# Kernel optimization log

Hardware: AMD Instinct MI355X
Metric: run time of the kernel (lower is better)

The kernel has to match this reference:

```python
import jax, jax.numpy as jnp
import numpy as np

NEG_SLOPE = 0.2  # PyG GATConv leaky_relu slope


def _seg_sum(x, seg, n):
    return jax.ops.segment_sum(x, seg, num_segments=n)


def _seg_softmax(e, seg, n):
    # numerically stable softmax over edges grouped by destination node
    m = jax.ops.segment_max(e, seg, num_segments=n)
    w = jnp.exp(e - m[seg])
    s = jax.ops.segment_sum(w, seg, num_segments=n)
    return w / (s[seg] + 1e-16)


def _gat_bipartite(x_src, x_dst, Ws, Wd, a_s, a_d, b, src, dst, H=4, C=32):
    # PyG GATConv((x_src, x_dst), edge_index), concat=True, add_self_loops=False
    n_dst = x_dst.shape[0]
    hs = (x_src @ Ws).reshape(-1, H, C)   # [Ns,H,C]
    hd = (x_dst @ Wd).reshape(-1, H, C)   # [Nd,H,C]
    es = jnp.einsum('nhc,hc->nh', hs, a_s)  # alpha_src per node
    ed = jnp.einsum('nhc,hc->nh', hd, a_d)  # alpha_dst per node
    e = jax.nn.leaky_relu(es[src] + ed[dst], NEG_SLOPE)  # [E,H]
    alpha = _seg_softmax(e, dst, n_dst)                   # softmax per dst
    out = _seg_sum(hs[src] * alpha[..., None], dst, n_dst)  # [Nd,H,C]
    return out.reshape(n_dst, H * C) + b


def _gcn_self_loops(x, W, b, src, dst):
    # PyG GCNConv with add_self_loops=True, symmetric normalization
    n = x.shape[0]
    xw = x @ W
    deg = _seg_sum(jnp.ones_like(dst, dtype=xw.dtype), dst, n) + 1.0  # +1 self loop
    dinv = jax.lax.rsqrt(deg)
    coef = (dinv[src] * dinv[dst])[:, None]
    agg = _seg_sum(xw[src] * coef, dst, n)
    agg = agg + xw * (dinv * dinv)[:, None]  # self-loop contribution
    return agg + b


def setup_inputs() -> dict:
    D, H, C = 128, 4, 32
    Nb, Nc, Nt = 200_000, 20_000, 2_000
    Eadj, Ebc, Ect = 1_600_000, 200_000, 20_000
    key = jax.random.key(0)
    ks = jax.random.split(key, 24)
    g = 1.0 / np.sqrt(D)
    ga = 1.0 / np.sqrt(C)
    inp = {
        'x_building': jax.random.normal(ks[0], (Nb, D), jnp.float32),
        'x_cable': jax.random.normal(ks[1], (Nc, D), jnp.float32),
        'x_transformer': jax.random.normal(ks[2], (Nt, D), jnp.float32),
        'Ws1': jax.random.normal(ks[3], (D, D), jnp.float32) * g,
        'Wd1': jax.random.normal(ks[4], (D, D), jnp.float32) * g,
        'a_s1': jax.random.normal(ks[5], (H, C), jnp.float32) * ga,
        'a_d1': jax.random.normal(ks[6], (H, C), jnp.float32) * ga,
        'b1': jnp.zeros((D,), jnp.float32),
        'Ws2': jax.random.normal(ks[7], (D, D), jnp.float32) * g,
        'Wd2': jax.random.normal(ks[8], (D, D), jnp.float32) * g,
        'a_s2': jax.random.normal(ks[9], (H, C), jnp.float32) * ga,
        'a_d2': jax.random.normal(ks[10], (H, C), jnp.float32) * ga,
        'b2': jnp.zeros((D,), jnp.float32),
        'Wg': jax.random.normal(ks[11], (D, D), jnp.float32) * g,
        'bg': jnp.zeros((D,), jnp.float32),
        'b2c_src': jax.random.randint(ks[12], (Ebc,), 0, Nb, jnp.int32),
        'b2c_dst': jax.random.randint(ks[13], (Ebc,), 0, Nc, jnp.int32),
        'c2t_src': jax.random.randint(ks[14], (Ect,), 0, Nc, jnp.int32),
        'c2t_dst': jax.random.randint(ks[15], (Ect,), 0, Nt, jnp.int32),
        'adj_src': jax.random.randint(ks[16], (Eadj,), 0, Nb, jnp.int32),
        'adj_dst': jax.random.randint(ks[17], (Eadj,), 0, Nb, jnp.int32),
    }
    return inp


def reference(x_building, x_cable, x_transformer,
              Ws1, Wd1, a_s1, a_d1, b1,
              Ws2, Wd2, a_s2, a_d2, b2,
              Wg, bg,
              b2c_src, b2c_dst, c2t_src, c2t_dst, adj_src, adj_dst):
    # building -> cable_group (GAT), residual 0.5
    h_lv = _gat_bipartite(x_building, x_cable, Ws1, Wd1, a_s1, a_d1, b1,
                          b2c_src, b2c_dst)
    h_cable = x_cable + 0.5 * h_lv
    # (updated) cable_group -> transformer (GAT), residual 0.5
    h_tr = _gat_bipartite(h_cable, x_transformer, Ws2, Wd2, a_s2, a_d2, b2,
                          c2t_src, c2t_dst)
    h_transformer = x_transformer + 0.5 * h_tr
    # building adjacency (GCN with self loops), residual 0.2
    h_adj = _gcn_self_loops(x_building, Wg, bg, adj_src, adj_dst)
    h_building = x_building + 0.2 * h_adj
    return (h_building, h_cable, h_transformer)
```

## Files before the change

kernel.cpp:

```cpp
#include <hip/hip_runtime.h>
#include <hip/hip_bf16.h>
#include <stdint.h>

typedef __attribute__((ext_vector_type(8))) short bf16x8;
typedef __attribute__((ext_vector_type(4))) float floatx4;
typedef __attribute__((ext_vector_type(4))) float f32x4;
typedef __attribute__((ext_vector_type(2))) float f32x2;

__device__ __forceinline__ float2 bf2f(uint32_t u) {
  float2 r;
  r.x = __uint_as_float(u << 16);
  r.y = __uint_as_float(u & 0xffff0000u);
  return r;
}
__device__ __forceinline__ uint16_t f2bf(float f) {
  uint32_t u = __float_as_uint(f);
  uint32_t r = (u + 0x7fffu + ((u >> 16) & 1u)) >> 16;
  return (uint16_t)r;
}
__device__ __forceinline__ uint32_t f2bf_pack(float a, float b) {
  return (uint32_t)f2bf(a) | ((uint32_t)f2bf(b) << 16);
}
__device__ __forceinline__ int iclamp(int v, int lo, int hi) {
  return v < lo ? lo : (v > hi ? hi : v);
}
__device__ __forceinline__ float lrelu(float v) { return v >= 0.f ? v : 0.2f * v; }

__device__ __forceinline__ int detect_f32(const uint32_t* __restrict__ det) {
  uint32_t v = det[threadIdx.x & 63];
  int e = (v >> 23) & 0xFF;
  unsigned long long b = __ballot(e >= 90 && e <= 160);
  return __popcll(b) >= 48;
}

__device__ __forceinline__ void acc8(float* a, uint4 r, float w) {
  float2 f0 = bf2f(r.x), f1 = bf2f(r.y), f2 = bf2f(r.z), f3 = bf2f(r.w);
  a[0] += w * f0.x; a[1] += w * f0.y;
  a[2] += w * f1.x; a[3] += w * f1.y;
  a[4] += w * f2.x; a[5] += w * f2.y;
  a[6] += w * f3.x; a[7] += w * f3.y;
}

__global__ void transp_zero(const void* __restrict__ W0, const void* __restrict__ W1,
                            const void* __restrict__ W2, const void* __restrict__ W3,
                            const void* __restrict__ W4, __hip_bfloat16* __restrict__ WT,
                            int* __restrict__ zp, int zn, const uint32_t* __restrict__ det) {
  int isf32 = detect_f32(det);
  int b = blockIdx.x;
  int w = b >> 6;
  int i = (b & 63) * 256 + threadIdx.x;
  const void* W = (w == 0) ? W0 : (w == 1) ? W1 : (w == 2) ? W2 : (w == 3) ? W3 : W4;
  int k = i >> 7, n = i & 127;
  uint16_t h;
  if (isf32)
    h = f2bf(((const float*)W)[i]);
  else
    h = ((const uint16_t*)W)[i];
  ((uint16_t*)WT)[w * 16384 + n * 128 + k] = h;
  for (int j = blockIdx.x * 256 + threadIdx.x; j < zn; j += gridDim.x * 256) zp[j] = 0;
}

__global__ void hist_all(const int* __restrict__ d0, int E0, const int* __restrict__ d1,
                         int E1, const int* __restrict__ d2, int E2,
                         int* __restrict__ cnt, int n0, int n1, int n2) {
  int i = blockIdx.x * 256 + threadIdx.x;
  if (i < E0) {
    atomicAdd(&cnt[iclamp(d0[i], 0, n0 - 1)], 1);
  } else if (i < E0 + E1) {
    int j = i - E0;
    atomicAdd(&cnt[n0 + iclamp(d1[j], 0, n1 - 1)], 1);
  } else if (i < E0 + E1 + E2) {
    int j = i - E0 - E1;
    atomicAdd(&cnt[n0 + n1 + iclamp(d2[j], 0, n2 - 1)], 1);
  }
}

__global__ void scanp_all(const int* __restrict__ cnt, int* __restrict__ off,
                          int* __restrict__ bsum, int n0, int n1, int n2,
                          int nb0, int nb1) {
  int b = blockIdx.x;
  int seg, lb, base, n;
  if (b < nb0) { seg = 0; lb = b; base = 0; n = n0; }
  else if (b < nb0 + nb1) { seg = 1; lb = b - nb0; base = n0; n = n1; }
  else { seg = 2; lb = b - nb0 - nb1; base = n0 + n1; n = n2; }
  const int* in = cnt + base;
  int* out = off + base;
  int* bs = bsum + seg * 256;
  __shared__ int lds[256];
  int t = threadIdx.x;
  int pbase = lb * 1024 + t * 4;
  int v[4];
  int s = 0;
#pragma unroll
  for (int j = 0; j < 4; j++) {
    v[j] = (pbase + j < n) ? in[pbase + j] : 0;
    s += v[j];
  }
  lds[t] = s;
  __syncthreads();
  for (int d = 1; d < 256; d <<= 1) {
    int x = 0;
    if (t >= d) x = lds[t - d];
    __syncthreads();
    if (t >= d) lds[t] += x;
    __syncthreads();
  }
  int run = (t > 0) ? lds[t - 1] : 0;
  if (t == 255) bs[lb] = lds[255];
#pragma unroll
  for (int j = 0; j < 4; j++) {
    if (pbase + j < n) out[pbase + j] = run;
    run += v[j];
  }
}

__global__ void scans_all(int* __restrict__ bsum, int nb0, int nb1, int nb2) {
  int seg = blockIdx.x;
  int nb = (seg == 0) ? nb0 : (seg == 1) ? nb1 : nb2;
  int* bs = bsum + seg * 256;
  __shared__ int lds[256];
  int t = threadIdx.x;
  int v = (t < nb) ? bs[t] : 0;
  lds[t] = v;
  __syncthreads();
  for (int d = 1; d < 256; d <<= 1) {
    int x = 0;
    if (t >= d) x = lds[t - d];
    __syncthreads();
    if (t >= d) lds[t] += x;
    __syncthreads();
  }
  if (t < nb) bs[t] = (t > 0) ? lds[t - 1] : 0;
}

__global__ void scanadd_dinv(int* __restrict__ off, const int* __restrict__ bsum,
                             const int* __restrict__ cnt, float* __restrict__ dinv,
                             int n0, int n1, int n2) {
  int i = blockIdx.x * 256 + threadIdx.x;
  if (i >= n0 + n1 + n2) return;
  int seg, li;
  if (i < n0) { seg = 0; li = i; }
  else if (i < n0 + n1) { seg = 1; li = i - n0; }
  else { seg = 2; li = i - n0 - n1; }
  off[i] += bsum[seg * 256 + (li >> 10)];
  if (seg == 2) dinv[li] = rsqrtf((float)max(cnt[i], 0) + 1.0f);
}

__global__ void fill_all(const int* __restrict__ s0, const int* __restrict__ d0, int E0,
                         const int* __restrict__ s1, const int* __restrict__ d1, int E1,
                         const int* __restrict__ s2, const int* __restrict__ d2, int E2,
                         const int* __restrict__ off, int* __restrict__ cur,
                         int* __restrict__ r0, int* __restrict__ r1, int* __restrict__ r2,
                         int n0, int n1, int n2) {
  int i = blockIdx.x * 256 + threadIdx.x;
  const int* sp;
  const int* dp;
  int* rp;
  int base, N, E, j;
  if (i < E0) { sp = s0; dp = d0; rp = r0; base = 0; N = n0; E = E0; j = i; }
  else if (i < E0 + E1) { sp = s1; dp = d1; rp = r1; base = n0; N = n1; E = E1; j = i - E0; }
  else if (i < E0 + E1 + E2) { sp = s2; dp = d2; rp = r2; base = n0 + n1; N = n2; E = E2; j = i - E0 - E1; }
  else return;
  int d = iclamp(dp[j], 0, N - 1);
  int gi = base + d;
  int p = off[gi] + atomicAdd(&cur[gi], 1);
  rp[iclamp(p, 0, E - 1)] = sp[j];
}

struct MMB {
  const void* A0; const void* A1; const void* A2;
  unsigned long long ao0, ao1, ao2;
  const __hip_bfloat16* W0; const __hip_bfloat16* W1; const __hip_bfloat16* W2;
  __hip_bfloat16* O0; __hip_bfloat16* O1; __hip_bfloat16* O2;
  float* E0; float* E1; float* E2;
  const void* V0; const void* V1; const void* V2;
  int M0, M1, M2, B1, B2;
};

__global__ __launch_bounds__(256) void mm_batch(MMB p, const uint32_t* __restrict__ det) {
  int isf32 = detect_f32(det);
  const void* Abase;
  size_t aoff;
  const __hip_bfloat16* WTp;
  __hip_bfloat16* out;
  float* esp;
  const void* av;
  int M, bRow;
  int bid = (int)blockIdx.x;
  if (bid >= p.B2) {
    Abase = p.A2; aoff = p.ao2; WTp = p.W2; out = p.O2; esp = p.E2; av = p.V2;
    M = p.M2; bRow = bid - p.B2;
  } else if (bid >= p.B1) {
    Abase = p.A1; aoff = p.ao1; WTp = p.W1; out = p.O1; esp = p.E1; av = p.V1;
    M = p.M1; bRow = bid - p.B1;
  } else {
    Abase = p.A0; aoff = p.ao0; WTp = p.W0; out = p.O0; esp = p.E0; av = p.V0;
    M = p.M0; bRow = bid;
  }
  __shared__ __align__(16) __hip_bfloat16 w[128 * 136];
  int tid = threadIdx.x;
  for (int i = tid; i < 2048; i += 256) {
    int row = i >> 4, ch = i & 15;
    *(uint4*)&w[row * 136 + ch * 8] = *(const uint4*)&WTp[row * 128 + ch * 8];
  }
  __syncthreads();
  int wave = tid >> 6, lane = tid & 63;
  int l15 = lane & 15, kq = (lane >> 4) * 8;
  int row0 = bRow * 64 + wave * 16;
  int m = row0 + l15;
  int mc = m < M ? m : M - 1;
  floatx4 acc[8];
#pragma unroll
  for (int t = 0; t < 8; t++) acc[t] = (floatx4){0.f, 0.f, 0.f, 0.f};
#pragma unroll
  for (int k0 = 0; k0 < 128; k0 += 32) {
    union { bf16x8 v; uint32_t u[4]; } au;
    size_t eoff = aoff + (size_t)mc * 128 + k0 + kq;
    if (isf32) {
      const f32x4* Af = (const f32x4*)((const float*)Abase + eoff);
      f32x4 f0 = __builtin_nontemporal_load(Af);
      f32x4 f1 = __builtin_nontemporal_load(Af + 1);
      au.u[0] = f2bf_pack(f0.x, f0.y);
      au.u[1] = f2bf_pack(f0.z, f0.w);
      au.u[2] = f2bf_pack(f1.x, f1.y);
      au.u[3] = f2bf_pack(f1.z, f1.w);
    } else {
      au.v = __builtin_nontemporal_load((const bf16x8*)((const __hip_bfloat16*)Abase + eoff));
    }
#pragma unroll
    for (int t = 0; t < 8; t++) {
      bf16x8 b = *(const bf16x8*)&w[(t * 16 + l15) * 136 + k0 + kq];
      acc[t] = __builtin_amdgcn_mfma_f32_16x16x32_bf16(au.v, b, acc[t], 0, 0, 0);
    }
  }
  int rbase = row0 + (lane >> 4) * 4;
  uint16_t* o16 = (uint16_t*)out;
#pragma unroll
  for (int r = 0; r < 4; r++) {
    int rr = rbase + r;
    if (rr < M) {
#pragma unroll
      for (int t = 0; t < 8; t++) o16[(size_t)rr * 128 + t * 16 + l15] = f2bf(acc[t][r]);
    }
  }
  if (esp) {
    float av8[8];
    if (isf32) {
      const float* af = (const float*)av;
#pragma unroll
      for (int t = 0; t < 8; t++) av8[t] = af[t * 16 + l15];
    } else {
      const uint16_t* ab = (const uint16_t*)av;
#pragma unroll
      for (int t = 0; t < 8; t++) av8[t] = __uint_as_float((uint32_t)ab[t * 16 + l15] << 16);
    }
    float ph[4][4];
#pragma unroll
    for (int h = 0; h < 4; h++)
#pragma unroll
      for (int r = 0; r < 4; r++)
        ph[h][r] = acc[2 * h][r] * av8[2 * h] + acc[2 * h + 1][r] * av8[2 * h + 1];
#pragma unroll
    for (int h = 0; h < 4; h++)
#pragma unroll
      for (int r = 0; r < 4; r++) {
        float v = ph[h][r];
        v += __shfl_xor(v, 1);
        v += __shfl_xor(v, 2);
        v += __shfl_xor(v, 4);
        v += __shfl_xor(v, 8);
        ph[h][r] = v;
      }
    int rr = l15 >> 2, hh = l15 & 3;
    float s0 = (hh == 0) ? ph[0][0] : (hh == 1) ? ph[1][0] : (hh == 2) ? ph[2][0] : ph[3][0];
    float s1 = (hh == 0) ? ph[0][1] : (hh == 1) ? ph[1][1] : (hh == 2) ? ph[2][1] : ph[3][1];
    float s2 = (hh == 0) ? ph[0][2] : (hh == 1) ? ph[1][2] : (hh == 2) ? ph[2][2] : ph[3][2];
    float s3 = (hh == 0) ? ph[0][3] : (hh == 1) ? ph[1][3] : (hh == 2) ? ph[2][3] : ph[3][3];
    float val = (rr == 0) ? s0 : (rr == 1) ? s1 : (rr == 2) ? s2 : s3;
    int rowA = row0 + (lane >> 4) * 4 + rr;
    if (rowA < M) esp[(size_t)rowA * 4 + hh] = val;
  }
}

__global__ __launch_bounds__(256) void gat_agg(
    const int* __restrict__ off, const int* __restrict__ cnt,
    const int* __restrict__ ssrc, const __hip_bfloat16* __restrict__ hs,
    const float* __restrict__ es, const float* __restrict__ ed,
    const void* __restrict__ xdst, const void* __restrict__ bias,
    void* __restrict__ outb, size_t ooff, int nt_out,
    int N, int Ns, int E, const uint32_t* __restrict__ det) {
  int isf32 = detect_f32(det);
  int wid = (blockIdx.x * 256 + threadIdx.x) >> 6;
  if (wid >= N) return;
  int lane = threadIdx.x & 63;
  int g = lane >> 4, il = lane & 15;
  int hh = il >> 2;
  int c8 = il * 8;
  int deg = iclamp(cnt[wid], 0, E);
  int o = iclamp(off[wid], 0, E - deg);
  const int* sp = ssrc + o;
  float edv = ed[wid * 4 + hh];
  float a[8] = {0.f, 0.f, 0.f, 0.f, 0.f, 0.f, 0.f, 0.f};
  float wsum = 0.f;
  for (int e = 0; e < deg; e += 8) {
    int e0 = e + g, e1 = e0 + 4;
    if (e1 < deg) {
      int s0 = iclamp(sp[e0], 0, Ns - 1);
      int s1 = iclamp(sp[e1], 0, Ns - 1);
      uint4 r0 = *(const uint4*)&hs[(size_t)s0 * 128 + c8];
      uint4 r1 = *(const uint4*)&hs[(size_t)s1 * 128 + c8];
      float w0 = __expf(lrelu(es[s0 * 4 + hh] + edv));
      float w1 = __expf(lrelu(es[s1 * 4 + hh] + edv));
      wsum += w0 + w1;
      acc8(a, r0, w0);
      acc8(a, r1, w1);
    } else if (e0 < deg) {
      int s0 = iclamp(sp[e0], 0, Ns - 1);
      uint4 r0 = *(const uint4*)&hs[(size_t)s0 * 128 + c8];
      float w0 = __expf(lrelu(es[s0 * 4 + hh] + edv));
      wsum += w0;
      acc8(a, r0, w0);
    }
  }
#pragma unroll
  for (int j = 0; j < 8; j++) {
    a[j] += __shfl_xor(a[j], 16);
    a[j] += __shfl_xor(a[j], 32);
  }
  wsum += __shfl_xor(wsum, 16);
  wsum += __shfl_xor(wsum, 32);
  float inv = 1.f / (wsum + 1e-16f);
  int cc = c8 + g * 2;
  float v0, v1;
  if (g == 0)      { v0 = a[0]; v1 = a[1]; }
  else if (g == 1) { v0 = a[2]; v1 = a[3]; }
  else if (g == 2) { v0 = a[4]; v1 = a[5]; }
  else             { v0 = a[6]; v1 = a[7]; }
  v0 *= inv; v1 *= inv;
  float x0, x1, b0, b1;
  if (isf32) {
    const float* xf = (const float*)xdst + (size_t)wid * 128 + cc;
    x0 = xf[0]; x1 = xf[1];
    const float* bf_ = (const float*)bias + cc;
    b0 = bf_[0]; b1 = bf_[1];
  } else {
    float2 xf = bf2f(*(const uint32_t*)&((const __hip_bfloat16*)xdst)[(size_t)wid * 128 + cc]);
    float2 bv = bf2f(*(const uint32_t*)&((const __hip_bfloat16*)bias)[cc]);
    x0 = xf.x; x1 = xf.y; b0 = bv.x; b1 = bv.y;
  }
  float r0 = x0 + 0.5f * (v0 + b0);
  float r1 = x1 + 0.5f * (v1 + b1);
  if (isf32) {
    f32x2* op = (f32x2*)((float*)outb + ooff + (size_t)wid * 128 + cc);
    f32x2 rv = {r0, r1};
    if (nt_out) __builtin_nontemporal_store(rv, op);
    else *op = rv;
  } else {
    *(uint32_t*)&((uint16_t*)outb)[ooff + (size_t)wid * 128 + cc] = f2bf_pack(r0, r1);
  }
}

__global__ __launch_bounds__(256) void gcn_agg(
    const int* __restrict__ off, const int* __restrict__ cnt,
    const int* __restrict__ ssrc, const __hip_bfloat16* __restrict__ xw,
    const float* __restrict__ dinv, const void* __restrict__ x,
    const void* __restrict__ bias, void* __restrict__ outb, size_t ooff,
    int N, int E, const uint32_t* __restrict__ det) {
  int isf32 = detect_f32(det);
  int wid = (blockIdx.x * 256 + threadIdx.x) >> 6;
  if (wid >= N) return;
  int lane = threadIdx.x & 63;
  int g = lane >> 4, il = lane & 15;
  int c8 = il * 8;
  int deg = iclamp(cnt[wid], 0, E);
  int o = iclamp(off[wid], 0, E - deg);
  const int* sp = ssrc + o;
  float di = dinv[wid];
  float a[8] = {0.f, 0.f, 0.f, 0.f, 0.f, 0.f, 0.f, 0.f};
  for (int e = 0; e < deg; e += 8) {
    int e0 = e + g, e1 = e0 + 4;
    if (e1 < deg) {
      int s0 = iclamp(sp[e0], 0, N - 1);
      int s1 = iclamp(sp[e1], 0, N - 1);
      uint4 r0 = *(const uint4*)&xw[(size_t)s0 * 128 + c8];
      uint4 r1 = *(const uint4*)&xw[(size_t)s1 * 128 + c8];
      float d0 = dinv[s0], d1 = dinv[s1];
      acc8(a, r0, d0);
      acc8(a, r1, d1);
    } else if (e0 < deg) {
      int s0 = iclamp(sp[e0], 0, N - 1);
      uint4 r0 = *(const uint4*)&xw[(size_t)s0 * 128 + c8];
      float d0 = dinv[s0];
      acc8(a, r0, d0);
    }
  }
  if (g == 0) {
    uint4 sr = *(const uint4*)&xw[(size_t)wid * 128 + c8];
    acc8(a, sr, di);
  }
#pragma unroll
  for (int j = 0; j < 8; j++) {
    a[j] += __shfl_xor(a[j], 16);
    a[j] += __shfl_xor(a[j], 32);
  }
  int cc = c8 + g * 2;
  float v0, v1;
  if (g == 0)      { v0 = a[0]; v1 = a[1]; }
  else if (g == 1) { v0 = a[2]; v1 = a[3]; }
  else if (g == 2) { v0 = a[4]; v1 = a[5]; }
  else             { v0 = a[6]; v1 = a[7]; }
  float agg0 = di * v0;
  float agg1 = di * v1;
  float x0, x1, b0, b1;
  if (isf32) {
    f32x2 xf = __builtin_nontemporal_load(
        (const f32x2*)((const float*)x + (size_t)wid * 128 + cc));
    x0 = xf.x; x1 = xf.y;
    const float* bf_ = (const float*)bias + cc;
    b0 = bf_[0]; b1 = bf_[1];
  } else {
    float2 xf = bf2f(*(const uint32_t*)&((const __hip_bfloat16*)x)[(size_t)wid * 128 + cc]);
    float2 bv = bf2f(*(const uint32_t*)&((const __hip_bfloat16*)bias)[cc]);
    x0 = xf.x; x1 = xf.y; b0 = bv.x; b1 = bv.y;
  }
  float r0 = x0 + 0.2f * (agg0 + b0);
  float r1 = x1 + 0.2f * (agg1 + b1);
  if (isf32) {
    f32x2 rv = {r0, r1};
    __builtin_nontemporal_store(rv, (f32x2*)((float*)outb + ooff + (size_t)wid * 128 + cc));
  } else {
    *(uint32_t*)&((uint16_t*)outb)[ooff + (size_t)wid * 128 + cc] = f2bf_pack(r0, r1);
  }
}

extern "C" void kernel_launch(void* const* d_in, const int* in_sizes, int n_in,
                              void* d_out, int out_size, void* d_ws, size_t ws_size,
                              hipStream_t stream) {
  const void* xb = d_in[0];
  const void* xc = d_in[1];
  const void* xt = d_in[2];
  const void* Ws1 = d_in[3];
  const void* Wd1 = d_in[4];
  const void* a_s1 = d_in[5];
  const void* a_d1 = d_in[6];
  const void* b1 = d_in[7];
  const void* Ws2 = d_in[8];
  const void* Wd2 = d_in[9];
  const void* a_s2 = d_in[10];
  const void* a_d2 = d_in[11];
  const void* b2 = d_in[12];
  const void* Wg = d_in[13];
  const void* bg = d_in[14];
  const int* b2c_src = (const int*)d_in[15];
  const int* b2c_dst = (const int*)d_in[16];
  const int* c2t_src = (const int*)d_in[17];
  const int* c2t_dst = (const int*)d_in[18];
  const int* adj_src = (const int*)d_in[19];
  const int* adj_dst = (const int*)d_in[20];

  const int Nb = in_sizes[0] / 128, Nc = in_sizes[1] / 128, Nt = in_sizes[2] / 128;
  const int Ebc = in_sizes[15], Ect = in_sizes[17], Eadj = in_sizes[19];
  const int nAll = Nc + Nt + Nb;
  const int Eall = Ebc + Ect + Eadj;

  auto al = [](size_t x) { return (x + 255) & ~(size_t)255; };
  char* base = (char*)d_ws;

  size_t o = 0;
  size_t o_WT = o;    o += al((size_t)5 * 16384 * 2);
  size_t o_cnt = o;   o += al((size_t)nAll * 4);
  size_t o_cur = o;   o += al((size_t)nAll * 4);
  size_t o_off = o;   o += al((size_t)nAll * 4);
  size_t o_dinv = o;  o += al((size_t)Nb * 4);
  size_t o_bsum = o;  o += al(3 * 256 * 4);
  size_t o_srtbc = o; o += al((size_t)Ebc * 4);
  size_t o_srtct = o; o += al((size_t)Ect * 4);
  size_t o_srtadj = o; o += al((size_t)Eadj * 4);
  size_t o_es1 = o;   o += al((size_t)Nb * 16);
  size_t o_ed1 = o;   o += al((size_t)Nc * 16);
  size_t o_es2 = o;   o += al((size_t)Nc * 16);
  size_t o_ed2 = o;   o += al((size_t)Nt * 16);
  size_t o_hd1 = o;   o += al((size_t)Nc * 256);
  size_t o_hd2 = o;   o += al((size_t)Nt * 256);
  size_t o_hs2 = o;   o += al((size_t)Nc * 256);
  size_t o_XW = o;    o += al((size_t)Nb * 256);
  if (o > ws_size) return;

  const uint32_t* det = (const uint32_t*)Ws1;
  __hip_bfloat16* WT = (__hip_bfloat16*)(base + o_WT);
  int* cnt = (int*)(base + o_cnt);
  int* cur = (int*)(base + o_cur);
  int* off = (int*)(base + o_off);
  float* dinv = (float*)(base + o_dinv);
  int* bsum = (int*)(base + o_bsum);
  int* srt_bc = (int*)(base + o_srtbc);
  int* srt_ct = (int*)(base + o_srtct);
  int* srt_adj = (int*)(base + o_srtadj);
  float* es1 = (float*)(base + o_es1);
  float* ed1 = (float*)(base + o_ed1);
  float* es2 = (float*)(base + o_es2);
  float* ed2 = (float*)(base + o_ed2);
  __hip_bfloat16* hd1 = (__hip_bfloat16*)(base + o_hd1);
  __hip_bfloat16* hd2 = (__hip_bfloat16*)(base + o_hd2);
  __hip_bfloat16* hs2 = (__hip_bfloat16*)(base + o_hs2);
  __hip_bfloat16* XW = (__hip_bfloat16*)(base + o_XW);

  const size_t off_b_out = 0;
  const size_t off_c_out = (size_t)Nb * 128;
  const size_t off_t_out = off_c_out + (size_t)Nc * 128;

  int* cnt_c = cnt;
  int* cnt_t = cnt + Nc;
  int* cnt_b = cnt + Nc + Nt;
  int* off_c = off;
  int* off_t = off + Nc;
  int* off_b = off + Nc + Nt;

  int zn = (int)((o_off - o_cnt) / 4);
  transp_zero<<<320, 256, 0, stream>>>(Ws1, Wd1, Ws2, Wd2, Wg, WT, cnt, zn, det);

  hist_all<<<(Eall + 255) / 256, 256, 0, stream>>>(b2c_dst, Ebc, c2t_dst, Ect, adj_dst,
                                                   Eadj, cnt, Nc, Nt, Nb);

  int nb0 = (Nc + 1023) / 1024, nb1 = (Nt + 1023) / 1024, nb2 = (Nb + 1023) / 1024;
  scanp_all<<<nb0 + nb1 + nb2, 256, 0, stream>>>(cnt, off, bsum, Nc, Nt, Nb, nb0, nb1);
  scans_all<<<3, 256, 0, stream>>>(bsum, nb0, nb1, nb2);
  scanadd_dinv<<<(nAll + 255) / 256, 256, 0, stream>>>(off, bsum, cnt, dinv, Nc, Nt, Nb);

  fill_all<<<(Eall + 255) / 256, 256, 0, stream>>>(b2c_src, b2c_dst, Ebc, c2t_src, c2t_dst,
                                                   Ect, adj_src, adj_dst, Eadj, off, cur,
                                                   srt_bc, srt_ct, srt_adj, Nc, Nt, Nb);

  {
    MMB p;
    p.A0 = xb; p.ao0 = 0; p.W0 = WT + 0 * 16384; p.O0 = XW; p.E0 = es1; p.V0 = a_s1; p.M0 = Nb;
    p.A1 = xc; p.ao1 = 0; p.W1 = WT + 1 * 16384; p.O1 = hd1; p.E1 = ed1; p.V1 = a_d1; p.M1 = Nc;
    p.A2 = xt; p.ao2 = 0; p.W2 = WT + 3 * 16384; p.O2 = hd2; p.E2 = ed2; p.V2 = a_d2; p.M2 = Nt;
    int g0 = (Nb + 63) / 64, g1 = (Nc + 63) / 64, g2 = (Nt + 63) / 64;
    p.B1 = g0; p.B2 = g0 + g1;
    mm_batch<<<g0 + g1 + g2, 256, 0, stream>>>(p, det);
  }

  gat_agg<<<(int)(((size_t)Nc * 64 + 255) / 256), 256, 0, stream>>>(
      off_c, cnt_c, srt_bc, XW, es1, ed1, xc, b1, d_out, off_c_out, 0, Nc, Nb, Ebc, det);

  {
    MMB p;
    p.A0 = d_out; p.ao0 = off_c_out; p.W0 = WT + 2 * 16384; p.O0 = hs2; p.E0 = es2;
    p.V0 = a_s2; p.M0 = Nc;
    p.A1 = xb; p.ao1 = 0; p.W1 = WT + 4 * 16384; p.O1 = XW; p.E1 = nullptr;
    p.V1 = nullptr; p.M1 = Nb;
    p.A2 = xb; p.ao2 = 0; p.W2 = WT; p.O2 = XW; p.E2 = nullptr; p.V2 = nullptr; p.M2 = 0;
    int g0 = (Nc + 63) / 64, g1 = (Nb + 63) / 64;
    p.B1 = g0; p.B2 = g0 + g1;
    mm_batch<<<g0 + g1, 256, 0, stream>>>(p, det);
  }

  gat_agg<<<(int)(((size_t)Nt * 64 + 255) / 256), 256, 0, stream>>>(
      off_t, cnt_t, srt_ct, hs2, es2, ed2, xt, b2, d_out, off_t_out, 1, Nt, Nc, Ect, det);

  gcn_agg<<<(int)(((size_t)Nb * 64 + 255) / 256), 256, 0, stream>>>(
      off_b, cnt_b, srt_adj, XW, dinv, xb, bg, d_out, off_b_out, Nb, Eadj, det);
}
```

Before: 628.9 us.

## Fuse CSR fill with projection GEMMs and co-schedule GCN with GAT aggregation

The edge-bucketing fill kernel now runs in the same launch as the first batched projection GEMM. When the workspace is large enough, the GCN weight projection is also computed in that first batch into a separate buffer. The GCN aggregation then runs in one launch alongside the first GAT aggregation, and the unused destination-projection outputs are no longer written. This removes kernel launches and tail idle time and overlaps independent work, at the cost of an extra Nb×128 bf16 workspace buffer and more branchy combined kernels.

```diff
diff --git a/kernel.cpp b/kernel.cpp
--- a/kernel.cpp
+++ b/kernel.cpp
@@ -146,39 +146,38 @@
   if (seg == 2) dinv[li] = rsqrtf((float)max(cnt[i], 0) + 1.0f);
 }
 
-__global__ void fill_all(const int* __restrict__ s0, const int* __restrict__ d0, int E0,
-                         const int* __restrict__ s1, const int* __restrict__ d1, int E1,
-                         const int* __restrict__ s2, const int* __restrict__ d2, int E2,
-                         const int* __restrict__ off, int* __restrict__ cur,
-                         int* __restrict__ r0, int* __restrict__ r1, int* __restrict__ r2,
-                         int n0, int n1, int n2) {
-  int i = blockIdx.x * 256 + threadIdx.x;
-  const int* sp;
-  const int* dp;
-  int* rp;
-  int base, N, E, j;
-  if (i < E0) { sp = s0; dp = d0; rp = r0; base = 0; N = n0; E = E0; j = i; }
-  else if (i < E0 + E1) { sp = s1; dp = d1; rp = r1; base = n0; N = n1; E = E1; j = i - E0; }
-  else if (i < E0 + E1 + E2) { sp = s2; dp = d2; rp = r2; base = n0 + n1; N = n2; E = E2; j = i - E0 - E1; }
-  else return;
-  int d = iclamp(dp[j], 0, N - 1);
-  int gi = base + d;
-  int p = off[gi] + atomicAdd(&cur[gi], 1);
-  rp[iclamp(p, 0, E - 1)] = sp[j];
-}
-
 struct MMB {
-  const void* A0; const void* A1; const void* A2;
-  unsigned long long ao0, ao1, ao2;
-  const __hip_bfloat16* W0; const __hip_bfloat16* W1; const __hip_bfloat16* W2;
-  __hip_bfloat16* O0; __hip_bfloat16* O1; __hip_bfloat16* O2;
-  float* E0; float* E1; float* E2;
-  const void* V0; const void* V1; const void* V2;
-  int M0, M1, M2, B1, B2;
+  const void *A0, *A1, *A2, *A3;
+  unsigned long long ao0, ao1, ao2, ao3;
+  const __hip_bfloat16 *W0, *W1, *W2, *W3;
+  __hip_bfloat16 *O0, *O1, *O2, *O3;
+  float *E0, *E1, *E2, *E3;
+  const void *V0, *V1, *V2, *V3;
+  int M0, M1, M2, M3;
+  int B1, B2, B3;
 };
 
-__global__ __launch_bounds__(256) void mm_batch(MMB p, const uint32_t* __restrict__ det) {
-  int isf32 = detect_f32(det);
+struct FillJ {
+  const int *s0, *d0, *s1, *d1, *s2, *d2;
+  int E0, E1, E2;
+  const int* off;
+  int* cur;
+  int *r0, *r1, *r2;
+  int n0, n1, n2;
+};
+
+struct AggJob {
+  const int* off; const int* cnt; const int* ssrc;
+  const __hip_bfloat16* tab;
+  const float* es; const float* ed;
+  const float* dinv;
+  const void* xdst; const void* bias;
+  void* outb;
+  unsigned long long ooff;
+  int nt_out, N, Ns, E, isGcn;
+};
+
+__device__ __forceinline__ void mm_body(const MMB& p, int bid, int isf32) {
   const void* Abase;
   size_t aoff;
   const __hip_bfloat16* WTp;
@@ -186,8 +185,10 @@
   float* esp;
   const void* av;
   int M, bRow;
-  int bid = (int)blockIdx.x;
-  if (bid >= p.B2) {
+  if (bid >= p.B3) {
+    Abase = p.A3; aoff = p.ao3; WTp = p.W3; out = p.O3; esp = p.E3; av = p.V3;
+    M = p.M3; bRow = bid - p.B3;
+  } else if (bid >= p.B2) {
     Abase = p.A2; aoff = p.ao2; WTp = p.W2; out = p.O2; esp = p.E2; av = p.V2;
     M = p.M2; bRow = bid - p.B2;
   } else if (bid >= p.B1) {
@@ -233,14 +234,16 @@
       acc[t] = __builtin_amdgcn_mfma_f32_16x16x32_bf16(au.v, b, acc[t], 0, 0, 0);
     }
   }
-  int rbase = row0 + (lane >> 4) * 4;
-  uint16_t* o16 = (uint16_t*)out;
-#pragma unroll
-  for (int r = 0; r < 4; r++) {
-    int rr = rbase + r;
-    if (rr < M) {
-#pragma unroll
-      for (int t = 0; t < 8; t++) o16[(size_t)rr * 128 + t * 16 + l15] = f2bf(acc[t][r]);
+  if (out) {
+    int rbase = row0 + (lane >> 4) * 4;
+    uint16_t* o16 = (uint16_t*)out;
+#pragma unroll
+    for (int r = 0; r < 4; r++) {
+      int rr = rbase + r;
+      if (rr < M) {
+#pragma unroll
+        for (int t = 0; t < 8; t++) o16[(size_t)rr * 128 + t * 16 + l15] = f2bf(acc[t][r]);
+      }
     }
   }
   if (esp) {
@@ -282,50 +285,69 @@
   }
 }
 
-__global__ __launch_bounds__(256) void gat_agg(
-    const int* __restrict__ off, const int* __restrict__ cnt,
-    const int* __restrict__ ssrc, const __hip_bfloat16* __restrict__ hs,
-    const float* __restrict__ es, const float* __restrict__ ed,
-    const void* __restrict__ xdst, const void* __restrict__ bias,
-    void* __restrict__ outb, size_t ooff, int nt_out,
-    int N, int Ns, int E, const uint32_t* __restrict__ det) {
+__device__ __forceinline__ void fill_body(const FillJ& f, int lb) {
+  int i = lb * 256 + (int)threadIdx.x;
+  const int* sp;
+  const int* dp;
+  int* rp;
+  int base, N, E, j;
+  if (i < f.E0) { sp = f.s0; dp = f.d0; rp = f.r0; base = 0; N = f.n0; E = f.E0; j = i; }
+  else if (i < f.E0 + f.E1) { sp = f.s1; dp = f.d1; rp = f.r1; base = f.n0; N = f.n1; E = f.E1; j = i - f.E0; }
+  else if (i < f.E0 + f.E1 + f.E2) { sp = f.s2; dp = f.d2; rp = f.r2; base = f.n0 + f.n1; N = f.n2; E = f.E2; j = i - f.E0 - f.E1; }
+  else return;
+  int d = iclamp(dp[j], 0, N - 1);
+  int gi = base + d;
+  int p = f.off[gi] + atomicAdd(&f.cur[gi], 1);
+  rp[iclamp(p, 0, E - 1)] = sp[j];
+}
+
+__global__ __launch_bounds__(256) void mm_fill(MMB p, FillJ f, int Gmm,
+                                               const uint32_t* __restrict__ det) {
   int isf32 = detect_f32(det);
-  int wid = (blockIdx.x * 256 + threadIdx.x) >> 6;
-  if (wid >= N) return;
+  int bid = (int)blockIdx.x;
+  if (bid < Gmm)
+    mm_body(p, bid, isf32);
+  else
+    fill_body(f, bid - Gmm);
+}
+
+__device__ __forceinline__ void gat_body(const AggJob& j, int lb, int isf32) {
+  int wid = (lb * 256 + (int)threadIdx.x) >> 6;
+  if (wid >= j.N) return;
   int lane = threadIdx.x & 63;
   int g = lane >> 4, il = lane & 15;
   int hh = il >> 2;
   int c8 = il * 8;
-  int deg = iclamp(cnt[wid], 0, E);
-  int o = iclamp(off[wid], 0, E - deg);
-  const int* sp = ssrc + o;
-  float edv = ed[wid * 4 + hh];
+  int deg = iclamp(j.cnt[wid], 0, j.E);
+  int o = iclamp(j.off[wid], 0, j.E - deg);
+  const int* sp = j.ssrc + o;
+  float edv = j.ed[wid * 4 + hh];
   float a[8] = {0.f, 0.f, 0.f, 0.f, 0.f, 0.f, 0.f, 0.f};
   float wsum = 0.f;
   for (int e = 0; e < deg; e += 8) {
     int e0 = e + g, e1 = e0 + 4;
     if (e1 < deg) {
-      int s0 = iclamp(sp[e0], 0, Ns - 1);
-      int s1 = iclamp(sp[e1], 0, Ns - 1);
-      uint4 r0 = *(const uint4*)&hs[(size_t)s0 * 128 + c8];
-      uint4 r1 = *(const uint4*)&hs[(size_t)s1 * 128 + c8];
-      float w0 = __expf(lrelu(es[s0 * 4 + hh] + edv));
-      float w1 = __expf(lrelu(es[s1 * 4 + hh] + edv));
+      int s0 = iclamp(sp[e0], 0, j.Ns - 1);
+      int s1 = iclamp(sp[e1], 0, j.Ns - 1);
+      uint4 r0 = *(const uint4*)&j.tab[(size_t)s0 * 128 + c8];
+      uint4 r1 = *(const uint4*)&j.tab[(size_t)s1 * 128 + c8];
+      float w0 = __expf(lrelu(j.es[s0 * 4 + hh] + edv));
+      float w1 = __expf(lrelu(j.es[s1 * 4 + hh] + edv));
       wsum += w0 + w1;
       acc8(a, r0, w0);
       acc8(a, r1, w1);
     } else if (e0 < deg) {
-      int s0 = iclamp(sp[e0], 0, Ns - 1);
-      uint4 r0 = *(const uint4*)&hs[(size_t)s0 * 128 + c8];
-      float w0 = __expf(lrelu(es[s0 * 4 + hh] + edv));
+      int s0 = iclamp(sp[e0], 0, j.Ns - 1);
+      uint4 r0 = *(const uint4*)&j.tab[(size_t)s0 * 128 + c8];
+      float w0 = __expf(lrelu(j.es[s0 * 4 + hh] + edv));
       wsum += w0;
       acc8(a, r0, w0);
     }
   }
 #pragma unroll
-  for (int j = 0; j < 8; j++) {
-    a[j] += __shfl_xor(a[j], 16);
-    a[j] += __shfl_xor(a[j], 32);
+  for (int q = 0; q < 8; q++) {
+    a[q] += __shfl_xor(a[q], 16);
+    a[q] += __shfl_xor(a[q], 32);
   }
   wsum += __shfl_xor(wsum, 16);
   wsum += __shfl_xor(wsum, 32);
@@ -339,69 +361,63 @@
   v0 *= inv; v1 *= inv;
   float x0, x1, b0, b1;
   if (isf32) {
-    const float* xf = (const float*)xdst + (size_t)wid * 128 + cc;
+    const float* xf = (const float*)j.xdst + (size_t)wid * 128 + cc;
     x0 = xf[0]; x1 = xf[1];
-    const float* bf_ = (const float*)bias + cc;
+    const float* bf_ = (const float*)j.bias + cc;
     b0 = bf_[0]; b1 = bf_[1];
   } else {
-    float2 xf = bf2f(*(const uint32_t*)&((const __hip_bfloat16*)xdst)[(size_t)wid * 128 + cc]);
-    float2 bv = bf2f(*(const uint32_t*)&((const __hip_bfloat16*)bias)[cc]);
+    float2 xf = bf2f(*(const uint32_t*)&((const __hip_bfloat16*)j.xdst)[(size_t)wid * 128 + cc]);
+    float2 bv = bf2f(*(const uint32_t*)&((const __hip_bfloat16*)j.bias)[cc]);
     x0 = xf.x; x1 = xf.y; b0 = bv.x; b1 = bv.y;
   }
   float r0 = x0 + 0.5f * (v0 + b0);
   float r1 = x1 + 0.5f * (v1 + b1);
   if (isf32) {
-    f32x2* op = (f32x2*)((float*)outb + ooff + (size_t)wid * 128 + cc);
+    f32x2* op = (f32x2*)((float*)j.outb + j.ooff + (size_t)wid * 128 + cc);
     f32x2 rv = {r0, r1};
-    if (nt_out) __builtin_nontemporal_store(rv, op);
+    if (j.nt_out) __builtin_nontemporal_store(rv, op);
     else *op = rv;
   } else {
-    *(uint32_t*)&((uint16_t*)outb)[ooff + (size_t)wid * 128 + cc] = f2bf_pack(r0, r1);
-  }
-}
-
-__global__ __launch_bounds__(256) void gcn_agg(
-    const int* __restrict__ off, const int* __restrict__ cnt,
-    const int* __restrict__ ssrc, const __hip_bfloat16* __restrict__ xw,
-    const float* __restrict__ dinv, const void* __restrict__ x,
-    const void* __restrict__ bias, void* __restrict__ outb, size_t ooff,
-    int N, int E, const uint32_t* __restrict__ det) {
-  int isf32 = detect_f32(det);
-  int wid = (blockIdx.x * 256 + threadIdx.x) >> 6;
-  if (wid >= N) return;
+    *(uint32_t*)&((uint16_t*)j.outb)[j.ooff + (size_t)wid * 128 + cc] = f2bf_pack(r0, r1);
+  }
+}
+
+__device__ __forceinline__ void gcn_body(const AggJob& j, int lb, int isf32) {
+  int wid = (lb * 256 + (int)threadIdx.x) >> 6;
+  if (wid >= j.N) return;
   int lane = threadIdx.x & 63;
   int g = lane >> 4, il = lane & 15;
   int c8 = il * 8;
-  int deg = iclamp(cnt[wid], 0, E);
-  int o = iclamp(off[wid], 0, E - deg);
-  const int* sp = ssrc + o;
-  float di = dinv[wid];
+  int deg = iclamp(j.cnt[wid], 0, j.E);
+  int o = iclamp(j.off[wid], 0, j.E - deg);
+  const int* sp = j.ssrc + o;
+  float di = j.dinv[wid];
   float a[8] = {0.f, 0.f, 0.f, 0.f, 0.f, 0.f, 0.f, 0.f};
   for (int e = 0; e < deg; e += 8) {
     int e0 = e + g, e1 = e0 + 4;
     if (e1 < deg) {
-      int s0 = iclamp(sp[e0], 0, N - 1);
-      int s1 = iclamp(sp[e1], 0, N - 1);
-      uint4 r0 = *(const uint4*)&xw[(size_t)s0 * 128 + c8];
-      uint4 r1 = *(const uint4*)&xw[(size_t)s1 * 128 + c8];
-      float d0 = dinv[s0], d1 = dinv[s1];
+      int s0 = iclamp(sp[e0], 0, j.Ns - 1);
+      int s1 = iclamp(sp[e1], 0, j.Ns - 1);
+      uint4 r0 = *(const uint4*)&j.tab[(size_t)s0 * 128 + c8];
+      uint4 r1 = *(const uint4*)&j.tab[(size_t)s1 * 128 + c8];
+      float d0 = j.dinv[s0], d1 = j.dinv[s1];
       acc8(a, r0, d0);
       acc8(a, r1, d1);
     } else if (e0 < deg) {
-      int s0 = iclamp(sp[e0], 0, N - 1);
-      uint4 r0 = *(const uint4*)&xw[(size_t)s0 * 128 + c8];
-      float d0 = dinv[s0];
+      int s0 = iclamp(sp[e0], 0, j.Ns - 1);
+      uint4 r0 = *(const uint4*)&j.tab[(size_t)s0 * 128 + c8];
+      float d0 = j.dinv[s0];
       acc8(a, r0, d0);
     }
   }
   if (g == 0) {
-    uint4 sr = *(const uint4*)&xw[(size_t)wid * 128 + c8];
+    uint4 sr = *(const uint4*)&j.tab[(size_t)wid * 128 + c8];
     acc8(a, sr, di);
   }
 #pragma unroll
-  for (int j = 0; j < 8; j++) {
-    a[j] += __shfl_xor(a[j], 16);
-    a[j] += __shfl_xor(a[j], 32);
+  for (int q = 0; q < 8; q++) {
+    a[q] += __shfl_xor(a[q], 16);
+    a[q] += __shfl_xor(a[q], 32);
   }
   int cc = c8 + g * 2;
   float v0, v1;
@@ -414,22 +430,36 @@
   float x0, x1, b0, b1;
   if (isf32) {
     f32x2 xf = __builtin_nontemporal_load(
-        (const f32x2*)((const float*)x + (size_t)wid * 128 + cc));
+        (const f32x2*)((const float*)j.xdst + (size_t)wid * 128 + cc));
     x0 = xf.x; x1 = xf.y;
-    const float* bf_ = (const float*)bias + cc;
+    const float* bf_ = (const float*)j.bias + cc;
     b0 = bf_[0]; b1 = bf_[1];
   } else {
-    float2 xf = bf2f(*(const uint32_t*)&((const __hip_bfloat16*)x)[(size_t)wid * 128 + cc]);
-    float2 bv = bf2f(*(const uint32_t*)&((const __hip_bfloat16*)bias)[cc]);
+    float2 xf = bf2f(*(const uint32_t*)&((const __hip_bfloat16*)j.xdst)[(size_t)wid * 128 + cc]);
+    float2 bv = bf2f(*(const uint32_t*)&((const __hip_bfloat16*)j.bias)[cc]);
     x0 = xf.x; x1 = xf.y; b0 = bv.x; b1 = bv.y;
   }
   float r0 = x0 + 0.2f * (agg0 + b0);
   float r1 = x1 + 0.2f * (agg1 + b1);
   if (isf32) {
     f32x2 rv = {r0, r1};
-    __builtin_nontemporal_store(rv, (f32x2*)((float*)outb + ooff + (size_t)wid * 128 + cc));
+    __builtin_nontemporal_store(rv, (f32x2*)((float*)j.outb + j.ooff + (size_t)wid * 128 + cc));
   } else {
-    *(uint32_t*)&((uint16_t*)outb)[ooff + (size_t)wid * 128 + cc] = f2bf_pack(r0, r1);
+    *(uint32_t*)&((uint16_t*)j.outb)[j.ooff + (size_t)wid * 128 + cc] = f2bf_pack(r0, r1);
+  }
+}
+
+__global__ __launch_bounds__(256) void agg_pair(AggJob j0, AggJob j1, int G0,
+                                                const uint32_t* __restrict__ det) {
+  int isf32 = detect_f32(det);
+  int bid = (int)blockIdx.x;
+  if (bid < G0) {
+    if (j0.isGcn) gcn_body(j0, bid, isf32);
+    else gat_body(j0, bid, isf32);
+  } else {
+    int lb = bid - G0;
+    if (j1.isGcn) gcn_body(j1, lb, isf32);
+    else gat_body(j1, lb, isf32);
   }
 }
 
@@ -462,29 +492,32 @@
   const int Ebc = in_sizes[15], Ect = in_sizes[17], Eadj = in_sizes[19];
   const int nAll = Nc + Nt + Nb;
   const int Eall = Ebc + Ect + Eadj;
+  const int BIG = 0x7fffffff;
 
   auto al = [](size_t x) { return (x + 255) & ~(size_t)255; };
   char* base = (char*)d_ws;
 
   size_t o = 0;
-  size_t o_WT = o;    o += al((size_t)5 * 16384 * 2);
-  size_t o_cnt = o;   o += al((size_t)nAll * 4);
-  size_t o_cur = o;   o += al((size_t)nAll * 4);
-  size_t o_off = o;   o += al((size_t)nAll * 4);
-  size_t o_dinv = o;  o += al((size_t)Nb * 4);
-  size_t o_bsum = o;  o += al(3 * 256 * 4);
-  size_t o_srtbc = o; o += al((size_t)Ebc * 4);
-  size_t o_srtct = o; o += al((size_t)Ect * 4);
+  size_t o_WT = o;     o += al((size_t)5 * 16384 * 2);
+  size_t o_cnt = o;    o += al((size_t)nAll * 4);
+  size_t o_cur = o;    o += al((size_t)nAll * 4);
+  size_t o_off = o;    o += al((size_t)nAll * 4);
+  size_t o_dinv = o;   o += al((size_t)Nb * 4);
+  size_t o_bsum = o;   o += al(3 * 256 * 4);
+  size_t o_srtbc = o;  o += al((size_t)Ebc * 4);
+  size_t o_srtct = o;  o += al((size_t)Ect * 4);
   size_t o_srtadj = o; o += al((size_t)Eadj * 4);
-  size_t o_es1 = o;   o += al((size_t)Nb * 16);
-  size_t o_ed1 = o;   o += al((size_t)Nc * 16);
-  size_t o_es2 = o;   o += al((size_t)Nc * 16);
-  size_t o_ed2 = o;   o += al((size_t)Nt * 16);
-  size_t o_hd1 = o;   o += al((size_t)Nc * 256);
-  size_t o_hd2 = o;   o += al((size_t)Nt * 256);
-  size_t o_hs2 = o;   o += al((size_t)Nc * 256);
-  size_t o_XW = o;    o += al((size_t)Nb * 256);
-  if (o > ws_size) return;
+  size_t o_es1 = o;    o += al((size_t)Nb * 16);
+  size_t o_ed1 = o;    o += al((size_t)Nc * 16);
+  size_t o_es2 = o;    o += al((size_t)Nc * 16);
+  size_t o_ed2 = o;    o += al((size_t)Nt * 16);
+  size_t o_hs2 = o;    o += al((size_t)Nc * 256);
+  size_t o_XW = o;     o += al((size_t)Nb * 256);
+  size_t endB = o;
+  size_t o_XWg = o;    o += al((size_t)Nb * 256);
+  size_t endA = o;
+  if (endB > ws_size) return;
+  const bool pathA = (endA <= ws_size);
 
   const uint32_t* det = (const uint32_t*)Ws1;
   __hip_bfloat16* WT = (__hip_bfloat16*)(base + o_WT);
@@ -500,10 +533,9 @@
   float* ed1 = (float*)(base + o_ed1);
   float* es2 = (float*)(base + o_es2);
   float* ed2 = (float*)(base + o_ed2);
-  __hip_bfloat16* hd1 = (__hip_bfloat16*)(base + o_hd1);
-  __hip_bfloat16* hd2 = (__hip_bfloat16*)(base + o_hd2);
   __hip_bfloat16* hs2 = (__hip_bfloat16*)(base + o_hs2);
   __hip_bfloat16* XW = (__hip_bfloat16*)(base + o_XW);
+  __hip_bfloat16* XWg = (__hip_bfloat16*)(base + o_XWg);
 
   const size_t off_b_out = 0;
   const size_t off_c_out = (size_t)Nb * 128;
@@ -527,38 +559,70 @@
   scans_all<<<3, 256, 0, stream>>>(bsum, nb0, nb1, nb2);
   scanadd_dinv<<<(nAll + 255) / 256, 256, 0, stream>>>(off, bsum, cnt, dinv, Nc, Nt, Nb);
 
-  fill_all<<<(Eall + 255) / 256, 256, 0, stream>>>(b2c_src, b2c_dst, Ebc, c2t_src, c2t_dst,
-                                                   Ect, adj_src, adj_dst, Eadj, off, cur,
-                                                   srt_bc, srt_ct, srt_adj, Nc, Nt, Nb);
+  FillJ fj;
+  fj.s0 = b2c_src; fj.d0 = b2c_dst; fj.s1 = c2t_src; fj.d1 = c2t_dst;
+  fj.s2 = adj_src; fj.d2 = adj_dst;
+  fj.E0 = Ebc; fj.E1 = Ect; fj.E2 = Eadj;
+  fj.off = off; fj.cur = cur;
+  fj.r0 = srt_bc; fj.r1 = srt_ct; fj.r2 = srt_adj;
+  fj.n0 = Nc; fj.n1 = Nt; fj.n2 = Nb;
+  int Gfill = (Eall + 255) / 256;
+
+  int g0 = (Nb + 63) / 64, g1 = (Nc + 63) / 64, g2 = (Nt + 63) / 64;
 
   {
     MMB p;
-    p.A0 = xb; p.ao0 = 0; p.W0 = WT + 0 * 16384; p.O0 = XW; p.E0 = es1; p.V0 = a_s1; p.M0 = Nb;
-    p.A1 = xc; p.ao1 = 0; p.W1 = WT + 1 * 16384; p.O1 = hd1; p.E1 = ed1; p.V1 = a_d1; p.M1 = Nc;
-    p.A2 = xt; p.ao2 = 0; p.W2 = WT + 3 * 16384; p.O2 = hd2; p.E2 = ed2; p.V2 = a_d2; p.M2 = Nt;
-    int g0 = (Nb + 63) / 64, g1 = (Nc + 63) / 64, g2 = (Nt + 63) / 64;
+    p.A0 = xb; p.ao0 = 0; p.W0 = WT + 0 * 16384; p.O0 = XW;      p.E0 = es1; p.V0 = a_s1; p.M0 = Nb;
+    p.A1 = xc; p.ao1 = 0; p.W1 = WT + 1 * 16384; p.O1 = nullptr; p.E1 = ed1; p.V1 = a_d1; p.M1 = Nc;
+    p.A2 = xt; p.ao2 = 0; p.W2 = WT + 3 * 16384; p.O2 = nullptr; p.E2 = ed2; p.V2 = a_d2; p.M2 = Nt;
+    p.A3 = xb; p.ao3 = 0; p.W3 = WT + 4 * 16384; p.O3 = XWg;     p.E3 = nullptr; p.V3 = nullptr; p.M3 = Nb;
     p.B1 = g0; p.B2 = g0 + g1;
-    mm_batch<<<g0 + g1 + g2, 256, 0, stream>>>(p, det);
-  }
-
-  gat_agg<<<(int)(((size_t)Nc * 64 + 255) / 256), 256, 0, stream>>>(
-      off_c, cnt_c, srt_bc, XW, es1, ed1, xc, b1, d_out, off_c_out, 0, Nc, Nb, Ebc, det);
-
-  {
+    p.B3 = pathA ? (g0 + g1 + g2) : BIG;
+    int Gmm = g0 + g1 + g2 + (pathA ? g0 : 0);
+    mm_fill<<<Gmm + Gfill, 256, 0, stream>>>(p, fj, Gmm, det);
+  }
+
+  AggJob ja1;
+  ja1.off = off_c; ja1.cnt = cnt_c; ja1.ssrc = srt_bc; ja1.tab = XW;
+  ja1.es = es1; ja1.ed = ed1; ja1.dinv = nullptr;
+  ja1.xdst = xc; ja1.bias = b1; ja1.outb = d_out; ja1.ooff = off_c_out;
+  ja1.nt_out = 0; ja1.N = Nc; ja1.Ns = Nb; ja1.E = Ebc; ja1.isGcn = 0;
+  int Ga1 = (Nc + 3) / 4;
+
+  AggJob jg;
+  jg.off = off_b; jg.cnt = cnt_b; jg.ssrc = srt_adj;
+  jg.tab = pathA ? XWg : XW;
+  jg.es = nullptr; jg.ed = nullptr; jg.dinv = dinv;
+  jg.xdst = xb; jg.bias = bg; jg.outb = d_out; jg.ooff = off_b_out;
+  jg.nt_out = 1; jg.N = Nb; jg.Ns = Nb; jg.E = Eadj; jg.isGcn = 1;
+  int Gg = (Nb + 3) / 4;
+
+  AggJob ja2;
+  ja2.off = off_t; ja2.cnt = cnt_t; ja2.ssrc = srt_ct; ja2.tab = hs2;
+  ja2.es = es2; ja2.ed = ed2; ja2.dinv = nullptr;
+  ja2.xdst = xt; ja2.bias = b2; ja2.outb = d_out; ja2.ooff = off_t_out;
+  ja2.nt_out = 1; ja2.N = Nt; ja2.Ns = Nc; ja2.E = Ect; ja2.isGcn = 0;
+  int Ga2 = (Nt + 3) / 4;
+
+  if (pathA) {
+    agg_pair<<<Gg + Ga1, 256, 0, stream>>>(jg, ja1, Gg, det);
     MMB p;
-    p.A0 = d_out; p.ao0 = off_c_out; p.W0 = WT + 2 * 16384; p.O0 = hs2; p.E0 = es2;
-    p.V0 = a_s2; p.M0 = Nc;
-    p.A1 = xb; p.ao1 = 0; p.W1 = WT + 4 * 16384; p.O1 = XW; p.E1 = nullptr;
-    p.V1 = nullptr; p.M1 = Nb;
-    p.A2 = xb; p.ao2 = 0; p.W2 = WT; p.O2 = XW; p.E2 = nullptr; p.V2 = nullptr; p.M2 = 0;
-    int g0 = (Nc + 63) / 64, g1 = (Nb + 63) / 64;
-    p.B1 = g0; p.B2 = g0 + g1;
-    mm_batch<<<g0 + g1, 256, 0, stream>>>(p, det);
-  }
-
-  gat_agg<<<(int)(((size_t)Nt * 64 + 255) / 256), 256, 0, stream>>>(
-      off_t, cnt_t, srt_ct, hs2, es2, ed2, xt, b2, d_out, off_t_out, 1, Nt, Nc, Ect, det);
-
-  gcn_agg<<<(int)(((size_t)Nb * 64 + 255) / 256), 256, 0, stream>>>(
-      off_b, cnt_b, srt_adj, XW, dinv, xb, bg, d_out, off_b_out, Nb, Eadj, det);
-}
+    p.A0 = d_out; p.ao0 = off_c_out; p.W0 = WT + 2 * 16384; p.O0 = hs2; p.E0 = es2; p.V0 = a_s2; p.M0 = Nc;
+    p.A1 = nullptr; p.ao1 = 0; p.W1 = nullptr; p.O1 = nullptr; p.E1 = nullptr; p.V1 = nullptr; p.M1 = 0;
+    p.A2 = nullptr; p.ao2 = 0; p.W2 = nullptr; p.O2 = nullptr; p.E2 = nullptr; p.V2 = nullptr; p.M2 = 0;
+    p.A3 = nullptr; p.ao3 = 0; p.W3 = nullptr; p.O3 = nullptr; p.E3 = nullptr; p.V3 = nullptr; p.M3 = 0;
+    p.B1 = BIG; p.B2 = BIG; p.B3 = BIG;
+    mm_fill<<<g1, 256, 0, stream>>>(p, fj, g1, det);
+    agg_pair<<<Ga2, 256, 0, stream>>>(ja2, ja2, Ga2, det);
+  } else {
+    agg_pair<<<Ga1, 256, 0, stream>>>(ja1, ja1, Ga1, det);
+    MMB p;
+    p.A0 = d_out; p.ao0 = off_c_out; p.W0 = WT + 2 * 16384; p.O0 = hs2; p.E0 = es2; p.V0 = a_s2; p.M0 = Nc;
+    p.A1 = xb; p.ao1 = 0; p.W1 = WT + 4 * 16384; p.O1 = XW; p.E1 = nullptr; p.V1 = nullptr; p.M1 = Nb;
+    p.A2 = nullptr; p.ao2 = 0; p.W2 = nullptr; p.O2 = nullptr; p.E2 = nullptr; p.V2 = nullptr; p.M2 = 0;
+    p.A3 = nullptr; p.ao3 = 0; p.W3 = nullptr; p.O3 = nullptr; p.E3 = nullptr; p.V3 = nullptr; p.M3 = 0;
+    p.B1 = g1; p.B2 = BIG; p.B3 = BIG;
+    mm_fill<<<g1 + g0, 256, 0, stream>>>(p, fj, g1 + g0, det);
+    agg_pair<<<Gg + Ga2, 256, 0, stream>>>(jg, ja2, Gg, det);
+  }
+}
```

New measurement: 609.8 us. 3.0% less time.
